# Kernel optimization log

Hardware: AMD Instinct MI355X
Metric: run time of the kernel (lower is better)

Reference implementation:

```python
import jax, jax.numpy as jnp
import numpy as np

N = 30000      # nodes
E = 480000     # edges per relation (avg degree 16)
H = 4          # GAT heads
D = 64         # out_size per head
F1, F2 = 256, 128   # per-metapath input feature dims
SIN = 256      # sen_in_size
HD = H * D     # 256, semantic-attention in_size
OUT = 64       # final out_size


def _gat(feat, src, dst, W, al, ar, b):
    """DGL GATConv (eval mode, dropout=0), activation=relu6."""
    h = (feat @ W).reshape(N, H, D)                     # [N,H,D]
    el = (h * al).sum(-1)                               # [N,H]
    er = (h * ar).sum(-1)                               # [N,H]
    e = jax.nn.leaky_relu(el[src] + er[dst], 0.2)       # [E,H]
    m = jax.ops.segment_max(e, dst, N)                  # edge-softmax over incoming edges
    p = jnp.exp(e - m[dst])
    s = jax.ops.segment_sum(p, dst, N)
    a = p / s[dst]                                      # [E,H]
    out = jax.ops.segment_sum(a[:, :, None] * h[src], dst, N)  # [N,H,D]
    out = out + b.reshape(1, H, D)
    return jnp.clip(out, 0.0, 6.0).reshape(N, H * D)    # relu6, flatten(1)


def _gcn_layer(x, src, dst, W, b):
    """DGL GraphConv, norm='both': D_in^{-1/2} A D_out^{-1/2} X W (+ b)."""
    ones = jnp.ones(src.shape[0], x.dtype)
    deg_o = jnp.clip(jax.ops.segment_sum(ones, src, N), 1.0, None)
    deg_i = jnp.clip(jax.ops.segment_sum(ones, dst, N), 1.0, None)
    h = (x @ W) * (deg_o[:, None] ** -0.5)
    h = jax.ops.segment_sum(h[src], dst, N) * (deg_i[:, None] ** -0.5)
    return h if b is None else h + b


def setup_inputs():
    key = jax.random.key(0)
    ks = jax.random.split(key, 28)
    f32 = jnp.float32
    nrm = lambda k, shp: jax.random.normal(k, shp, f32) * 0.05
    ri = lambda k, shp: jax.random.randint(k, shp, 0, N, jnp.int32)
    return dict(
        feat0=jax.random.normal(ks[0], (N, F1), f32),
        feat1=jax.random.normal(ks[1], (N, F2), f32),
        sen_feat=jax.random.normal(ks[2], (N, SIN), f32),
        Wgat0=nrm(ks[11], (F1, H * D)), al0=nrm(ks[12], (H, D)), ar0=nrm(ks[13], (H, D)), b0=nrm(ks[14], (H * D,)),
        Wgat1=nrm(ks[15], (F2, H * D)), al1=nrm(ks[16], (H, D)), ar1=nrm(ks[17], (H, D)), b1=nrm(ks[18], (H * D,)),
        Wp1=nrm(ks[19], (HD, OUT)), bp1=nrm(ks[20], (OUT,)), wp2=nrm(ks[21], (OUT,)),
        Wf=nrm(ks[22], (HD, OUT)), bf=nrm(ks[23], (OUT,)),
        Wg1=nrm(ks[24], (SIN, OUT)), bg1=nrm(ks[25], (OUT,)), Wg2=nrm(ks[26], (OUT, OUT)),
        src0=ri(ks[3], (E,)), dst0=ri(ks[4], (E,)),
        src1=ri(ks[5], (E,)), dst1=ri(ks[6], (E,)),
        gsrc=ri(ks[7], (E,)), gdst=ri(ks[8], (E,)),
        asrc=ri(ks[9], (E,)), adst=ri(ks[10], (E,)),
        k=10,
    )


def reference(feat0, feat1, sen_feat,
              Wgat0, al0, ar0, b0, Wgat1, al1, ar1, b1,
              Wp1, bp1, wp2, Wf, bf, Wg1, bg1, Wg2,
              src0, dst0, src1, dst1, gsrc, gdst, asrc, adst, k):
    # per-metapath GAT embeddings
    z0 = _gat(feat0, src0, dst0, Wgat0, al0, ar0, b0)   # [N, HD]
    z1 = _gat(feat1, src1, dst1, Wgat1, al1, ar1, b1)   # [N, HD]
    z = jnp.stack([z0, z1], axis=1)                     # [N, M=2, HD]
    # PathAttention (semantic attention over metapaths)
    w = jnp.tanh(z @ Wp1 + bp1) @ wp2                   # [N, M]
    beta = jax.nn.softmax(w.mean(0))                    # [M]
    fused = jnp.einsum('m,nmf->nf', beta, z)            # [N, HD]
    Femb = fused @ Wf + bf                              # [N, OUT]
    # two-layer GCN on the sentence graph
    p1 = jnp.tanh(_gcn_layer(sen_feat, gsrc, gdst, Wg1, bg1))
    P = _gcn_layer(p1, gsrc, gdst, Wg2, None)           # [N, OUT]
    # spectral loss: fuse embeddings, trace of Laplacian quadratic form on first k dims
    Z = 0.5 * (Femb + P)                                # [N, OUT]
    Zk = Z[:, :k]
    diff = Zk[asrc] - Zk[adst]
    tr = 0.5 * jnp.sum(diff * diff)                     # tr(Zk^T (D - A) Zk)
    return (tr, Z)
```

## Files before the change

kernel.cpp:

```cpp
#include <hip/hip_runtime.h>
#include <math.h>

#define NN 30000
#define NE 480000
#define NBLK 118
#define NMT 235
#define NTRB 7500
#define CAPD 128

typedef unsigned short ushort_t;
typedef unsigned int uint_t;
typedef __attribute__((ext_vector_type(8))) short short8;
typedef __attribute__((ext_vector_type(4))) float f32x4;

__device__ __forceinline__ ushort_t f2bf(float x) {
  uint_t u = __float_as_uint(x);
  u = (u + 0x7FFF + ((u >> 16) & 1)) >> 16;
  return (ushort_t)u;
}
__device__ __forceinline__ float bf2f(ushort_t v) {
  return __uint_as_float(((uint_t)v) << 16);
}

__device__ __forceinline__ float wred(float v) {
#pragma unroll
  for (int off = 32; off > 0; off >>= 1) v += __shfl_xor(v, off);
  return v;
}

__global__ void prep_kernel(float4* __restrict__ zp, const float* __restrict__ W0,
                            const float* __restrict__ W1, const float* __restrict__ W2,
                            const float* __restrict__ W3, const float* __restrict__ W4,
                            ushort_t* __restrict__ T0, ushort_t* __restrict__ T1,
                            ushort_t* __restrict__ T2, ushort_t* __restrict__ T3,
                            ushort_t* __restrict__ T4, const float* __restrict__ F0,
                            const float* __restrict__ F1, ushort_t* __restrict__ B0,
                            ushort_t* __restrict__ B1) {
  int id = blockIdx.x * 256 + threadIdx.x;
  if (id < 52501) {
    zp[id] = make_float4(0.f, 0.f, 0.f, 0.f);
    return;
  }
  int wid = id - 52501;
  if (wid < 147456) {
    const float* W;
    ushort_t* T;
    int K, N, base;
    if (wid < 65536) { W = W0; T = T0; K = 256; N = 256; base = 0; }
    else if (wid < 98304) { W = W1; T = T1; K = 128; N = 256; base = 65536; }
    else if (wid < 114688) { W = W2; T = T2; K = 256; N = 64; base = 98304; }
    else if (wid < 131072) { W = W3; T = T3; K = 256; N = 64; base = 114688; }
    else { W = W4; T = T4; K = 256; N = 64; base = 131072; }
    int l = wid - base;
    int k = l / N, n = l - k * N;
    T[(size_t)n * K + k] = f2bf(W[l]);
    return;
  }
  int cid = wid - 147456;
  const float* S;
  ushort_t* D;
  if (cid < 960000) { S = F0; D = B0; }
  else {
    cid -= 960000;
    if (cid >= 480000) return;
    S = F1; D = B1;
  }
  const float4* p = (const float4*)(S + (size_t)cid * 8);
  float4 a = p[0], b = p[1];
  short8 o;
  o[0] = (short)f2bf(a.x); o[1] = (short)f2bf(a.y);
  o[2] = (short)f2bf(a.z); o[3] = (short)f2bf(a.w);
  o[4] = (short)f2bf(b.x); o[5] = (short)f2bf(b.y);
  o[6] = (short)f2bf(b.z); o[7] = (short)f2bf(b.w);
  *(short8*)(D + (size_t)cid * 8) = o;
}


__device__ __forceinline__ void mfma_core_f32(const float* __restrict__ A0,
                                              const ushort_t* __restrict__ BT, int K, int bm,
                                              short* __restrict__ As, short* __restrict__ Bs,
                                              f32x4 acc[2][4]) {
  int tid = threadIdx.x;
  int lane = tid & 63, w = tid >> 6;
  int q = lane >> 4, mr = lane & 15;
#pragma unroll 1
  for (int k0 = 0; k0 < K; k0 += 32) {
    {
      int r = tid >> 1, hf = tid & 1;
      int gr = bm + r;
      float4 f0 = make_float4(0.f, 0.f, 0.f, 0.f), f1 = f0, f2 = f0, f3 = f0;
      if (gr < NN) {
        const float4* pa = (const float4*)(A0 + (size_t)gr * K + k0 + hf * 16);
        f0 = pa[0]; f1 = pa[1]; f2 = pa[2]; f3 = pa[3];
      }
      short8 lo, hi;
      lo[0] = (short)f2bf(f0.x); lo[1] = (short)f2bf(f0.y);
      lo[2] = (short)f2bf(f0.z); lo[3] = (short)f2bf(f0.w);
      lo[4] = (short)f2bf(f1.x); lo[5] = (short)f2bf(f1.y);
      lo[6] = (short)f2bf(f1.z); lo[7] = (short)f2bf(f1.w);
      hi[0] = (short)f2bf(f2.x); hi[1] = (short)f2bf(f2.y);
      hi[2] = (short)f2bf(f2.z); hi[3] = (short)f2bf(f2.w);
      hi[4] = (short)f2bf(f3.x); hi[5] = (short)f2bf(f3.y);
      hi[6] = (short)f2bf(f3.z); hi[7] = (short)f2bf(f3.w);
      short* dst = As + r * 40 + hf * 16;
      *(short8*)(dst) = lo;
      *(short8*)(dst + 8) = hi;
    }
    {
      int n = tid >> 2, qk = tid & 3;
      short8 bv = *(const short8*)((const short*)BT + (size_t)n * K + k0 + qk * 8);
      *(short8*)(Bs + n * 40 + qk * 8) = bv;
    }
    __syncthreads();
    short8 a0 = *(short8*)(As + (w * 32 + mr) * 40 + q * 8);
    short8 a1 = *(short8*)(As + (w * 32 + 16 + mr) * 40 + q * 8);
#pragma unroll
    for (int j = 0; j < 4; ++j) {
      short8 b = *(short8*)(Bs + (j * 16 + mr) * 40 + q * 8);
      acc[0][j] = __builtin_amdgcn_mfma_f32_16x16x32_bf16(a0, b, acc[0][j], 0, 0, 0);
      acc[1][j] = __builtin_amdgcn_mfma_f32_16x16x32_bf16(a1, b, acc[1][j], 0, 0, 0);
    }
    __syncthreads();
  }
}

__device__ __forceinline__ void mfma_core2_bfK(const ushort_t* __restrict__ A0,
                                               const ushort_t* __restrict__ BT, int K, int bm,
                                               short* __restrict__ As, short* __restrict__ Bs,
                                               f32x4 acc[2][8]) {
  int tid = threadIdx.x;
  int lane = tid & 63, w = tid >> 6;
  int q = lane >> 4, mr = lane & 15;
#pragma unroll 1
  for (int k0 = 0; k0 < K; k0 += 32) {
    {
      int r = tid >> 1, hf = tid & 1;
      int gr = bm + r;
      short8 v0 = {0, 0, 0, 0, 0, 0, 0, 0}, v1 = v0;
      if (gr < NN) {
        const short* p0 = (const short*)A0 + (size_t)gr * K + k0 + hf * 16;
        v0 = *(const short8*)p0;
        v1 = *(const short8*)(p0 + 8);
      }
      short* dst = As + r * 40 + hf * 16;
      *(short8*)(dst) = v0;
      *(short8*)(dst + 8) = v1;
    }
    {
      int n = tid >> 1, qk = tid & 1;
      const short* src = (const short*)BT + (size_t)n * K + k0 + qk * 16;
      short8 b0 = *(const short8*)src;
      short8 b1 = *(const short8*)(src + 8);
      short* d = Bs + n * 40 + qk * 16;
      *(short8*)d = b0;
      *(short8*)(d + 8) = b1;
    }
    __syncthreads();
    short8 a0 = *(short8*)(As + (w * 32 + mr) * 40 + q * 8);
    short8 a1 = *(short8*)(As + (w * 32 + 16 + mr) * 40 + q * 8);
#pragma unroll
    for (int j = 0; j < 8; ++j) {
      short8 b = *(short8*)(Bs + (j * 16 + mr) * 40 + q * 8);
      acc[0][j] = __builtin_amdgcn_mfma_f32_16x16x32_bf16(a0, b, acc[0][j], 0, 0, 0);
      acc[1][j] = __builtin_amdgcn_mfma_f32_16x16x32_bf16(a1, b, acc[1][j], 0, 0, 0);
    }
    __syncthreads();
  }
}

__global__ __launch_bounds__(256) void mfma_all_kernel(
    const ushort_t* __restrict__ fB0, const ushort_t* __restrict__ fB1,
    const float* __restrict__ sen, const ushort_t* __restrict__ WT0,
    const ushort_t* __restrict__ WT1, const ushort_t* __restrict__ Wg1T,
    ushort_t* __restrict__ h0, ushort_t* __restrict__ h1, ushort_t* __restrict__ gcnA,
    const float* __restrict__ al0, const float* __restrict__ ar0, float* __restrict__ el0,
    float* __restrict__ er0, const float* __restrict__ al1, const float* __restrict__ ar1,
    float* __restrict__ el1, float* __restrict__ er1, const float* __restrict__ rdo) {
  __shared__ short As[128 * 40];
  __shared__ short Bs[128 * 40];
  int y = blockIdx.y;
  int bm = blockIdx.x * 128;
  int lane = threadIdx.x & 63, w = threadIdx.x >> 6;
  int q = lane >> 4, mr = lane & 15;
  if (y < 4) {
    int gsel = y >> 1, p = y & 1;
    const ushort_t* A = gsel ? fB1 : fB0;
    int K = gsel ? 128 : 256;
    const ushort_t* WT = gsel ? WT1 : WT0;
    ushort_t* H = gsel ? h1 : h0;
    const float* al = gsel ? al1 : al0;
    const float* ar = gsel ? ar1 : ar0;
    float* el = gsel ? el1 : el0;
    float* er = gsel ? er1 : er0;
    f32x4 acc[2][8];
#pragma unroll
    for (int i = 0; i < 2; ++i)
#pragma unroll
      for (int j = 0; j < 8; ++j) acc[i][j] = (f32x4){0.f, 0.f, 0.f, 0.f};
    mfma_core2_bfK(A, WT + (size_t)p * 128 * K, K, bm, As, Bs, acc);
    float alv[8], arv[8];
#pragma unroll
    for (int j = 0; j < 8; ++j) {
      alv[j] = al[p * 128 + j * 16 + mr];
      arv[j] = ar[p * 128 + j * 16 + mr];
    }
#pragma unroll
    for (int i = 0; i < 2; ++i)
#pragma unroll
      for (int r = 0; r < 4; ++r) {
        int gr = bm + w * 32 + i * 16 + q * 4 + r;
        float pl0 = 0.f, pr0 = 0.f, pl1 = 0.f, pr1 = 0.f;
#pragma unroll
        for (int j = 0; j < 4; ++j) {
          pl0 = fmaf(acc[i][j][r], alv[j], pl0);
          pr0 = fmaf(acc[i][j][r], arv[j], pr0);
          pl1 = fmaf(acc[i][j + 4][r], alv[j + 4], pl1);
          pr1 = fmaf(acc[i][j + 4][r], arv[j + 4], pr1);
        }
#pragma unroll
        for (int m = 1; m < 16; m <<= 1) {
          pl0 += __shfl_xor(pl0, m);
          pr0 += __shfl_xor(pr0, m);
          pl1 += __shfl_xor(pl1, m);
          pr1 += __shfl_xor(pr1, m);
        }
        if (gr < NN) {
          if (mr == 0) {
            el[gr * 4 + 2 * p] = pl0;
            er[gr * 4 + 2 * p] = pr0;
            el[gr * 4 + 2 * p + 1] = pl1;
            er[gr * 4 + 2 * p + 1] = pr1;
          }
#pragma unroll
          for (int j = 0; j < 8; ++j)
            H[(size_t)gr * 256 + p * 128 + j * 16 + mr] = f2bf(acc[i][j][r]);
        }
      }
  } else {
    f32x4 acc[2][4];
#pragma unroll
    for (int i = 0; i < 2; ++i)
#pragma unroll
      for (int j = 0; j < 4; ++j) acc[i][j] = (f32x4){0.f, 0.f, 0.f, 0.f};
    mfma_core_f32(sen, Wg1T, 256, bm, As, Bs, acc);
#pragma unroll
    for (int i = 0; i < 2; ++i)
#pragma unroll
      for (int r = 0; r < 4; ++r) {
        int gr = bm + w * 32 + i * 16 + q * 4 + r;
        if (gr < NN) {
          float sc = rdo[gr];
#pragma unroll
          for (int j = 0; j < 4; ++j)
            gcnA[(size_t)gr * 64 + j * 16 + mr] = f2bf(acc[i][j][r] * sc);
        }
      }
  }
}

__global__ __launch_bounds__(256) void mfma_attnwf_kernel(
    const ushort_t* __restrict__ z0, const ushort_t* __restrict__ z1,
    const ushort_t* __restrict__ WpfT, const float* __restrict__ bp1,
    const float* __restrict__ wp2, float* __restrict__ pbuf, ushort_t* __restrict__ Y0,
    ushort_t* __restrict__ Y1) {
  __shared__ short As[128 * 40];
  __shared__ short Bs[128 * 40];
  __shared__ float wsum[4];
  const ushort_t* A = blockIdx.y ? z1 : z0;
  ushort_t* Y = blockIdx.y ? Y1 : Y0;
  int bm = blockIdx.x * 128;
  f32x4 acc[2][8];
#pragma unroll
  for (int i = 0; i < 2; ++i)
#pragma unroll
    for (int j = 0; j < 8; ++j) acc[i][j] = (f32x4){0.f, 0.f, 0.f, 0.f};
  mfma_core2_bfK(A, WpfT, 256, bm, As, Bs, acc);
  int lane = threadIdx.x & 63, w = threadIdx.x >> 6;
  int q = lane >> 4, mr = lane & 15;
  float local = 0.f;
#pragma unroll
  for (int j = 0; j < 4; ++j) {
    int col = j * 16 + mr;
    float bp = bp1[col], wp = wp2[col];
#pragma unroll
    for (int i = 0; i < 2; ++i)
#pragma unroll
      for (int r = 0; r < 4; ++r) {
        int gr = bm + w * 32 + i * 16 + q * 4 + r;
        if (gr < NN) local += tanhf(acc[i][j][r] + bp) * wp;
      }
  }
  local = wred(local);
  if (lane == 0) wsum[w] = local;
#pragma unroll
  for (int j = 4; j < 8; ++j) {
    int col = (j - 4) * 16 + mr;
#pragma unroll
    for (int i = 0; i < 2; ++i)
#pragma unroll
      for (int r = 0; r < 4; ++r) {
        int gr = bm + w * 32 + i * 16 + q * 4 + r;
        if (gr < NN) Y[(size_t)gr * 64 + col] = f2bf(acc[i][j][r]);
      }
  }
  __syncthreads();
  if (threadIdx.x == 0)
    pbuf[blockIdx.y * NMT + blockIdx.x] = wsum[0] + wsum[1] + wsum[2] + wsum[3];
}

__global__ void hist_kernel(const int* __restrict__ d0, const int* __restrict__ d1,
                            const int* __restrict__ d2, const int* __restrict__ d3,
                            int* __restrict__ cnt) {
  int g = blockIdx.y;
  const int* d = g == 0 ? d0 : g == 1 ? d1 : g == 2 ? d2 : d3;
  int e = blockIdx.x * 256 + threadIdx.x;
  if (e < NE) atomicAdd(&cnt[g * NN + d[e]], 1);
}

__global__ __launch_bounds__(256) void scan_blocks_kernel(const int* __restrict__ cnt,
                                                          int* __restrict__ rows,
                                                          int* __restrict__ bsum) {
  __shared__ int sm[256];
  int g = blockIdx.y, t = threadIdx.x;
  int i = blockIdx.x * 256 + t;
  int v = (i < NN) ? cnt[g * NN + i] : 0;
  sm[t] = v;
  __syncthreads();
#pragma unroll
  for (int off = 1; off < 256; off <<= 1) {
    int tmp = (t >= off) ? sm[t - off] : 0;
    __syncthreads();
    sm[t] += tmp;
    __syncthreads();
  }
  if (i < NN) rows[g * (NN + 1) + i] = sm[t] - v;
  if (t == 255) bsum[g * NBLK + blockIdx.x] = sm[255];
}

__global__ __launch_bounds__(128) void scan_tops_kernel(int* __restrict__ bsum,
                                                        int* __restrict__ boff) {
  __shared__ int sm[128];
  int g = blockIdx.y, t = threadIdx.x;
  int v = (t < NBLK) ? bsum[g * NBLK + t] : 0;
  sm[t] = v;
  __syncthreads();
#pragma unroll
  for (int off = 1; off < 128; off <<= 1) {
    int tmp = (t >= off) ? sm[t - off] : 0;
    __syncthreads();
    sm[t] += tmp;
    __syncthreads();
  }
  if (t < NBLK) boff[g * NBLK + t] = sm[t] - v;
}

__global__ void add_off_kernel(int* __restrict__ rows, const int* __restrict__ boff) {
  int g = blockIdx.y, t = threadIdx.x;
  int i = blockIdx.x * 256 + t;
  if (i < NN) rows[g * (NN + 1) + i] += boff[g * NBLK + blockIdx.x];
  if (blockIdx.x == 0 && t == 0) rows[g * (NN + 1) + NN] = NE;
}

__global__ void scatter_kernel(const int* __restrict__ s0, const int* __restrict__ s1,
                               const int* __restrict__ s2, const int* __restrict__ d0,
                               const int* __restrict__ d1, const int* __restrict__ d2,
                               const int* __restrict__ rows, int* __restrict__ cnt2,
                               int* __restrict__ cols, const int* __restrict__ cnt_deg,
                               float* __restrict__ rdo, float* __restrict__ rdi,
                               const int* __restrict__ rows_g) {
  int g = blockIdx.y;
  if (g == 3) {
    int n = blockIdx.x * 256 + threadIdx.x;
    if (n < NN) {
      rdo[n] = rsqrtf(fmaxf((float)cnt_deg[n], 1.f));
      float di = (float)(rows_g[n + 1] - rows_g[n]);
      rdi[n] = rsqrtf(fmaxf(di, 1.f));
    }
    return;
  }
  const int* sp = g == 0 ? s0 : g == 1 ? s1 : s2;
  const int* dp = g == 0 ? d0 : g == 1 ? d1 : d2;
  int e = blockIdx.x * 256 + threadIdx.x;
  if (e >= NE) return;
  int d = dp[e];
  int pos = rows[g * (NN + 1) + d] + atomicAdd(&cnt2[g * NN + d], 1);
  cols[(size_t)g * NE + pos] = sp[e];
}

__global__ __launch_bounds__(256) void gat_node_kernel(
    const int* __restrict__ rows0, const int* __restrict__ cols0, const float* __restrict__ el0,
    const float* __restrict__ er0, const ushort_t* __restrict__ h0,
    const float* __restrict__ bias0, ushort_t* __restrict__ zz0, const int* __restrict__ rows1,
    const int* __restrict__ cols1, const float* __restrict__ el1, const float* __restrict__ er1,
    const ushort_t* __restrict__ h1, const float* __restrict__ bias1,
    ushort_t* __restrict__ zz1) {
  __shared__ float aw[4][CAPD][4];
  int g = blockIdx.y;
  const int* rows = g ? rows1 : rows0;
  const int* cols = g ? cols1 : cols0;
  const float* el = g ? el1 : el0;
  const float* er = g ? er1 : er0;
  const ushort_t* h = g ? h1 : h0;
  const float* bias = g ? bias1 : bias0;
  ushort_t* z = g ? zz1 : zz0;

  int lane = threadIdx.x & 63, w = threadIdx.x >> 6;
  int n = blockIdx.x * 4 + w;
  int r0 = rows[n], r1 = rows[n + 1];
  int deg = r1 - r0;
  float4 er4 = *(const float4*)&er[n * 4];
  float s0 = 0.f, s1 = 0.f, s2 = 0.f, s3 = 0.f;
  for (int j = lane; j < deg; j += 64) {
    int s = cols[r0 + j];
    float4 elv = *(const float4*)&el[s * 4];
    float v0 = elv.x + er4.x; v0 = v0 > 0.f ? v0 : 0.2f * v0;
    float v1 = elv.y + er4.y; v1 = v1 > 0.f ? v1 : 0.2f * v1;
    float v2 = elv.z + er4.z; v2 = v2 > 0.f ? v2 : 0.2f * v2;
    float v3 = elv.w + er4.w; v3 = v3 > 0.f ? v3 : 0.2f * v3;
    float e0 = __expf(v0), e1 = __expf(v1), e2 = __expf(v2), e3 = __expf(v3);
    s0 += e0; s1 += e1; s2 += e2; s3 += e3;
    if (j < CAPD) {
      aw[w][j][0] = e0; aw[w][j][1] = e1; aw[w][j][2] = e2; aw[w][j][3] = e3;
    }
  }
  s0 = wred(s0); s1 = wred(s1); s2 = wred(s2); s3 = wred(s3);
  __syncthreads();
  int hh = lane >> 4;
  float denom = hh == 0 ? s0 : hh == 1 ? s1 : hh == 2 ? s2 : s3;
  float myer = hh == 0 ? er4.x : hh == 1 ? er4.y : hh == 2 ? er4.z : er4.w;
  float invd = (deg > 0) ? 1.f / denom : 0.f;
  float4 acc = make_float4(0.f, 0.f, 0.f, 0.f);
  int jc = deg < CAPD ? deg : CAPD;
  for (int j = 0; j < jc; j += 16) {
    int si[16];
    float ai[16];
#pragma unroll
    for (int t = 0; t < 16; ++t) {
      int jj = j + t;
      int jx = jj < jc ? jj : jc - 1;
      si[t] = cols[r0 + jx];
      ai[t] = (jj < jc) ? aw[w][jj][hh] : 0.f;
    }
    ushort4 ui[16];
#pragma unroll
    for (int t = 0; t < 16; ++t) ui[t] = *(const ushort4*)&h[(size_t)si[t] * 256 + lane * 4];
#pragma unroll
    for (int t = 0; t < 16; ++t) {
      acc.x = fmaf(ai[t], bf2f(ui[t].x), acc.x);
      acc.y = fmaf(ai[t], bf2f(ui[t].y), acc.y);
      acc.z = fmaf(ai[t], bf2f(ui[t].z), acc.z);
      acc.w = fmaf(ai[t], bf2f(ui[t].w), acc.w);
    }
  }
  for (int j = jc; j < deg; ++j) {
    int s = cols[r0 + j];
    float v = el[s * 4 + hh] + myer;
    v = v > 0.f ? v : 0.2f * v;
    float a = __expf(v);
    ushort4 hu = *(const ushort4*)&h[(size_t)s * 256 + lane * 4];
    acc.x = fmaf(a, bf2f(hu.x), acc.x);
    acc.y = fmaf(a, bf2f(hu.y), acc.y);
    acc.z = fmaf(a, bf2f(hu.z), acc.z);
    acc.w = fmaf(a, bf2f(hu.w), acc.w);
  }
  float4 bv = *(const float4*)&bias[lane * 4];
  ushort4 o;
  o.x = f2bf(fminf(fmaxf(acc.x * invd + bv.x, 0.f), 6.f));
  o.y = f2bf(fminf(fmaxf(acc.y * invd + bv.y, 0.f), 6.f));
  o.z = f2bf(fminf(fmaxf(acc.z * invd + bv.z, 0.f), 6.f));
  o.w = f2bf(fminf(fmaxf(acc.w * invd + bv.w, 0.f), 6.f));
  *(ushort4*)&z[(size_t)n * 256 + lane * 4] = o;
}

__global__ __launch_bounds__(256) void gcn_gather12_kernel(
    const int* __restrict__ rows, const int* __restrict__ cols, const ushort_t* __restrict__ X,
    const float* __restrict__ rdi, const float* __restrict__ bg1, const float* __restrict__ Wg2,
    const float* __restrict__ rdo, ushort_t* __restrict__ out2, const float* __restrict__ pbuf,
    float* __restrict__ wb) {
  __shared__ float psm[4][64];
  int lane = threadIdx.x & 63, w = threadIdx.x >> 6;
  if (blockIdx.x == 0) {
    __shared__ float sm[8];
    int t = threadIdx.x;
    float a0 = 0.f, a1 = 0.f;
    for (int i = t; i < NMT; i += 256) {
      a0 += pbuf[i];
      a1 += pbuf[NMT + i];
    }
    a0 = wred(a0);
    a1 = wred(a1);
    if (lane == 0) { sm[w] = a0; sm[4 + w] = a1; }
    __syncthreads();
    if (t == 0) {
      float w0 = (sm[0] + sm[1] + sm[2] + sm[3]) * (1.0f / NN);
      float w1 = (sm[4] + sm[5] + sm[6] + sm[7]) * (1.0f / NN);
      float mx = fmaxf(w0, w1);
      float e0 = expf(w0 - mx), e1 = expf(w1 - mx);
      float inv = 1.f / (e0 + e1);
      wb[2] = e0 * inv;
      wb[3] = e1 * inv;
    }
  }
  int n = blockIdx.x * 4 + w;
  if (n >= NN) return;
  int r0 = rows[n], r1 = rows[n + 1];
  int eg = lane >> 4, fl = lane & 15;
  float facc[4] = {0.f, 0.f, 0.f, 0.f};
  for (int j = r0; j < r1; j += 16) {
    int si[4];
    float sel[4];
#pragma unroll
    for (int t = 0; t < 4; ++t) {
      int jj = j + 4 * t + eg;
      int jx = jj < r1 ? jj : r1 - 1;
      si[t] = cols[jx];
      sel[t] = (jj < r1) ? 1.f : 0.f;
    }
    ushort4 xv[4];
#pragma unroll
    for (int t = 0; t < 4; ++t) xv[t] = *(const ushort4*)&X[(size_t)si[t] * 64 + fl * 4];
#pragma unroll
    for (int t = 0; t < 4; ++t) {
      facc[0] = fmaf(sel[t], bf2f(xv[t].x), facc[0]);
      facc[1] = fmaf(sel[t], bf2f(xv[t].y), facc[1]);
      facc[2] = fmaf(sel[t], bf2f(xv[t].z), facc[2]);
      facc[3] = fmaf(sel[t], bf2f(xv[t].w), facc[3]);
    }
  }
#pragma unroll
  for (int u = 0; u < 4; ++u) {
    facc[u] += __shfl_xor(facc[u], 16);
    facc[u] += __shfl_xor(facc[u], 32);
  }
  if (eg == 0) *(float4*)&psm[w][fl * 4] = make_float4(facc[0], facc[1], facc[2], facc[3]);
  __syncthreads();
  float p = tanhf(psm[w][lane] * rdi[n] + bg1[lane]);
  float o = 0.f;
#pragma unroll
  for (int k = 0; k < 64; ++k) o = fmaf(__shfl(p, k), Wg2[k * 64 + lane], o);
  out2[(size_t)n * 64 + lane] = f2bf(o * rdo[n]);
}

__global__ __launch_bounds__(256) void gcn_gather2_kernel(
    const int* __restrict__ rows, const int* __restrict__ cols, const ushort_t* __restrict__ X,
    const float* __restrict__ rdi, const ushort_t* __restrict__ Y0,
    const ushort_t* __restrict__ Y1, const float* __restrict__ wb, const float* __restrict__ bf,
    const int* __restrict__ kptr, float* __restrict__ Zc, float* __restrict__ dout) {
  int lane = threadIdx.x & 63, w = threadIdx.x >> 6;
  int n = blockIdx.x * 4 + w;
  if (n >= NN) return;
  int r0 = rows[n], r1 = rows[n + 1];
  int eg = lane >> 4, fl = lane & 15;
  float facc[4] = {0.f, 0.f, 0.f, 0.f};
  for (int j = r0; j < r1; j += 16) {
    int si[4];
    float sel[4];
#pragma unroll
    for (int t = 0; t < 4; ++t) {
      int jj = j + 4 * t + eg;
      int jx = jj < r1 ? jj : r1 - 1;
      si[t] = cols[jx];
      sel[t] = (jj < r1) ? 1.f : 0.f;
    }
    ushort4 xv[4];
#pragma unroll
    for (int t = 0; t < 4; ++t) xv[t] = *(const ushort4*)&X[(size_t)si[t] * 64 + fl * 4];
#pragma unroll
    for (int t = 0; t < 4; ++t) {
      facc[0] = fmaf(sel[t], bf2f(xv[t].x), facc[0]);
      facc[1] = fmaf(sel[t], bf2f(xv[t].y), facc[1]);
      facc[2] = fmaf(sel[t], bf2f(xv[t].z), facc[2]);
      facc[3] = fmaf(sel[t], bf2f(xv[t].w), facc[3]);
    }
  }
#pragma unroll
  for (int u = 0; u < 4; ++u) {
    facc[u] += __shfl_xor(facc[u], 16);
    facc[u] += __shfl_xor(facc[u], 32);
  }
  if (eg == 0) {
    float ri = rdi[n];
    ushort4 y0 = *(const ushort4*)&Y0[(size_t)n * 64 + fl * 4];
    ushort4 y1 = *(const ushort4*)&Y1[(size_t)n * 64 + fl * 4];
    float4 bfv = *(const float4*)&bf[fl * 4];
    float w2 = wb[2], w3 = wb[3];
    float zv[4];
    zv[0] = 0.5f * (w2 * bf2f(y0.x) + w3 * bf2f(y1.x) + bfv.x + facc[0] * ri);
    zv[1] = 0.5f * (w2 * bf2f(y0.y) + w3 * bf2f(y1.y) + bfv.y + facc[1] * ri);
    zv[2] = 0.5f * (w2 * bf2f(y0.z) + w3 * bf2f(y1.z) + bfv.z + facc[2] * ri);
    zv[3] = 0.5f * (w2 * bf2f(y0.w) + w3 * bf2f(y1.w) + bfv.w + facc[3] * ri);
    float* dp = dout + 1 + (size_t)n * 64 + fl * 4;
    dp[0] = zv[0]; dp[1] = zv[1]; dp[2] = zv[2]; dp[3] = zv[3];
    int k = *kptr;
    if (fl < 4) {
      float4 zk;
      zk.x = (fl * 4 + 0 < k) ? zv[0] : 0.f;
      zk.y = (fl * 4 + 1 < k) ? zv[1] : 0.f;
      zk.z = (fl * 4 + 2 < k) ? zv[2] : 0.f;
      zk.w = (fl * 4 + 3 < k) ? zv[3] : 0.f;
      *(float4*)&Zc[(size_t)n * 16 + fl * 4] = zk;
    }
  }
}

__global__ __launch_bounds__(256) void tr_kernel(const int* __restrict__ asrc,
                                                 const int* __restrict__ adst,
                                                 const int* __restrict__ kptr,
                                                 const float* __restrict__ Zc,
                                                 const float* __restrict__ dout,
                                                 float* __restrict__ trbuf) {
  __shared__ float wsum[4];
  int lane = threadIdx.x & 63, w = threadIdx.x >> 6;
  int k = *kptr;
  int eg = lane >> 2, c0 = (lane & 3) * 4;
  int e = blockIdx.x * 64 + w * 16 + eg;
  float local = 0.f;
  if (e < NE) {
    int a = asrc[e], b = adst[e];
    if (k <= 16) {
      float4 za = *(const float4*)&Zc[(size_t)a * 16 + c0];
      float4 zb = *(const float4*)&Zc[(size_t)b * 16 + c0];
      float dx = za.x - zb.x, dy = za.y - zb.y, dz = za.z - zb.z, dw = za.w - zb.w;
      local = dx * dx + dy * dy + dz * dz + dw * dw;
    } else {
      const float* Za = dout + 1 + (size_t)a * 64;
      const float* Zb = dout + 1 + (size_t)b * 64;
#pragma unroll
      for (int st = 0; st < 4; ++st) {
#pragma unroll
        for (int t = 0; t < 4; ++t) {
          int c = c0 + st * 16 + t;
          if (c < k) {
            float d2 = Za[c] - Zb[c];
            local += d2 * d2;
          }
        }
      }
    }
  }
#pragma unroll
  for (int off = 32; off > 0; off >>= 1) local += __shfl_down(local, off);
  if (lane == 0) wsum[w] = local;
  __syncthreads();
  if (threadIdx.x == 0) trbuf[blockIdx.x] = wsum[0] + wsum[1] + wsum[2] + wsum[3];
}

__global__ __launch_bounds__(256) void tr_reduce_kernel(const float* __restrict__ trbuf,
                                                        float* __restrict__ dout) {
  __shared__ float sm[4];
  int t = threadIdx.x;
  float a = 0.f;
  for (int i = t; i < NTRB; i += 256) a += trbuf[i];
  a = wred(a);
  int lane = t & 63, w = t >> 6;
  if (lane == 0) sm[w] = a;
  __syncthreads();
  if (t == 0) dout[0] = 0.5f * (sm[0] + sm[1] + sm[2] + sm[3]);
}

extern "C" void kernel_launch(void* const* d_in, const int* in_sizes, int n_in, void* d_out,
                              int out_size, void* d_ws, size_t ws_size, hipStream_t stream) {
  const float* feat0 = (const float*)d_in[0];
  const float* feat1 = (const float*)d_in[1];
  const float* sen = (const float*)d_in[2];
  const float* Wgat0 = (const float*)d_in[3];
  const float* al0 = (const float*)d_in[4];
  const float* ar0 = (const float*)d_in[5];
  const float* b0 = (const float*)d_in[6];
  const float* Wgat1 = (const float*)d_in[7];
  const float* al1 = (const float*)d_in[8];
  const float* ar1 = (const float*)d_in[9];
  const float* b1 = (const float*)d_in[10];
  const float* Wp1 = (const float*)d_in[11];
  const float* bp1 = (const float*)d_in[12];
  const float* wp2 = (const float*)d_in[13];
  const float* Wf = (const float*)d_in[14];
  const float* bf = (const float*)d_in[15];
  const float* Wg1 = (const float*)d_in[16];
  const float* bg1 = (const float*)d_in[17];
  const float* Wg2 = (const float*)d_in[18];
  const int* src0 = (const int*)d_in[19];
  const int* dst0 = (const int*)d_in[20];
  const int* src1 = (const int*)d_in[21];
  const int* dst1 = (const int*)d_in[22];
  const int* gsrc = (const int*)d_in[23];
  const int* gdst = (const int*)d_in[24];
  const int* asrc = (const int*)d_in[25];
  const int* adst = (const int*)d_in[26];
  const int* kptr = (const int*)d_in[27];
  float* out = (float*)d_out;
  float* ws = (float*)d_ws;

  float* wb = ws;
  int* cnt = (int*)(ws + 4);
  int* cnt2 = (int*)(ws + 120004);
  float* rdo = ws + 210004;
  float* rdi = ws + 240004;
  int* rows = (int*)(ws + 270004);
  int* bsum = (int*)(ws + 360008);
  int* boff = (int*)(ws + 360364);
  int* cols = (int*)(ws + 360720);
  float* el0 = ws + 1800720;
  float* er0 = ws + 1920720;
  float* el1 = ws + 2040720;
  float* er1 = ws + 2160720;
  float* pbuf = ws + 2280720;
  float* trbuf = el0;
  ushort_t* h0 = (ushort_t*)(ws + 2283068);
  ushort_t* h1 = (ushort_t*)(ws + 6123068);
  ushort_t* z0 = (ushort_t*)(ws + 9963068);
  ushort_t* z1 = (ushort_t*)(ws + 13803068);
  ushort_t* gcnA = (ushort_t*)(ws + 17643068);
  ushort_t* gcnA2 = (ushort_t*)(ws + 18603068);
  ushort_t* Y0 = (ushort_t*)(ws + 19563068);
  ushort_t* Y1 = (ushort_t*)(ws + 20523068);
  ushort_t* WT0 = (ushort_t*)(ws + 21483068);
  ushort_t* WT1 = (ushort_t*)(ws + 21515836);
  ushort_t* WpfT = (ushort_t*)(ws + 21532220);
  ushort_t* Wg1T = (ushort_t*)(ws + 21548604);
  float* Zc = ws + 21556796;

  int* rows_g = rows + 2 * (NN + 1);
  int* cols_g = cols + 2 * NE;
  int* cnt_deg = cnt + 3 * NN;

  ushort_t* fB0 = z0;
  ushort_t* fB1 = z1;

  prep_kernel<<<6407, 256, 0, stream>>>((float4*)ws, Wgat0, Wgat1, Wp1, Wf, Wg1, WT0, WT1, WpfT,
                                        WpfT + 16384, Wg1T, feat0, feat1, fB0, fB1);

  hist_kernel<<<dim3(1875, 4), 256, 0, stream>>>(dst0, dst1, gdst, gsrc, cnt);
  scan_blocks_kernel<<<dim3(NBLK, 3), 256, 0, stream>>>(cnt, rows, bsum);
  scan_tops_kernel<<<dim3(1, 3), 128, 0, stream>>>(bsum, boff);
  add_off_kernel<<<dim3(NBLK, 3), 256, 0, stream>>>(rows, boff);
  scatter_kernel<<<dim3(1875, 4), 256, 0, stream>>>(src0, src1, gsrc, dst0, dst1, gdst, rows,
                                                    cnt2, cols, cnt_deg, rdo, rdi, rows_g);

  mfma_all_kernel<<<dim3(NMT, 5), 256, 0, stream>>>(fB0, fB1, sen, WT0, WT1, Wg1T, h0, h1,
                                                    gcnA, al0, ar0, el0, er0, al1, ar1, el1,
                                                    er1, rdo);

  gat_node_kernel<<<dim3(7500, 2), 256, 0, stream>>>(rows, cols, el0, er0, h0, b0, z0,
                                                     rows + (NN + 1), cols + NE, el1, er1, h1,
                                                     b1, z1);

  mfma_attnwf_kernel<<<dim3(NMT, 2), 256, 0, stream>>>(z0, z1, WpfT, bp1, wp2, pbuf, Y0, Y1);

  gcn_gather12_kernel<<<7500, 256, 0, stream>>>(rows_g, cols_g, gcnA, rdi, bg1, Wg2, rdo, gcnA2,
                                                pbuf, wb);
  gcn_gather2_kernel<<<7500, 256, 0, stream>>>(rows_g, cols_g, gcnA2, rdi, Y0, Y1, wb, bf, kptr,
                                               Zc, out);

  tr_kernel<<<NTRB, 256, 0, stream>>>(asrc, adst, kptr, Zc, out, trbuf);
  tr_reduce_kernel<<<1, 256, 0, stream>>>(trbuf, out);
}
```

Measured before the change: 515.7 us.

## Merge attention GEMM with first GCN gather; widen GAT gather loads

The GAT node aggregation now splits each wave into two halves, each handling alternating edges with 16-byte bf16 loads of 8 features per lane, then combines the halves with a cross-half shuffle. The semantic-attention MFMA GEMM and the first GCN gather/transform are merged into one heterogeneous launch, since they are independent. The softmax over metapath scores is recomputed redundantly per wave in the final gather kernel instead of by a special block. This removes a launch and a global handoff through wb, and lets the GEMM blocks overlap the gather blocks. In exchange, every wave repeats the small pbuf reduction.

After: 537.9 us. +4.3%, slower.

```diff
diff --git a/kernel.cpp b/kernel.cpp
--- a/kernel.cpp
+++ b/kernel.cpp
@@ -21,6 +21,8 @@
 __device__ __forceinline__ float bf2f(ushort_t v) {
   return __uint_as_float(((uint_t)v) << 16);
 }
+__device__ __forceinline__ float bflo(uint_t d) { return __uint_as_float(d << 16); }
+__device__ __forceinline__ float bfhi(uint_t d) { return __uint_as_float(d & 0xFFFF0000u); }
 
 __device__ __forceinline__ float wred(float v) {
 #pragma unroll
@@ -258,56 +260,6 @@
   }
 }
 
-__global__ __launch_bounds__(256) void mfma_attnwf_kernel(
-    const ushort_t* __restrict__ z0, const ushort_t* __restrict__ z1,
-    const ushort_t* __restrict__ WpfT, const float* __restrict__ bp1,
-    const float* __restrict__ wp2, float* __restrict__ pbuf, ushort_t* __restrict__ Y0,
-    ushort_t* __restrict__ Y1) {
-  __shared__ short As[128 * 40];
-  __shared__ short Bs[128 * 40];
-  __shared__ float wsum[4];
-  const ushort_t* A = blockIdx.y ? z1 : z0;
-  ushort_t* Y = blockIdx.y ? Y1 : Y0;
-  int bm = blockIdx.x * 128;
-  f32x4 acc[2][8];
-#pragma unroll
-  for (int i = 0; i < 2; ++i)
-#pragma unroll
-    for (int j = 0; j < 8; ++j) acc[i][j] = (f32x4){0.f, 0.f, 0.f, 0.f};
-  mfma_core2_bfK(A, WpfT, 256, bm, As, Bs, acc);
-  int lane = threadIdx.x & 63, w = threadIdx.x >> 6;
-  int q = lane >> 4, mr = lane & 15;
-  float local = 0.f;
-#pragma unroll
-  for (int j = 0; j < 4; ++j) {
-    int col = j * 16 + mr;
-    float bp = bp1[col], wp = wp2[col];
-#pragma unroll
-    for (int i = 0; i < 2; ++i)
-#pragma unroll
-      for (int r = 0; r < 4; ++r) {
-        int gr = bm + w * 32 + i * 16 + q * 4 + r;
-        if (gr < NN) local += tanhf(acc[i][j][r] + bp) * wp;
-      }
-  }
-  local = wred(local);
-  if (lane == 0) wsum[w] = local;
-#pragma unroll
-  for (int j = 4; j < 8; ++j) {
-    int col = (j - 4) * 16 + mr;
-#pragma unroll
-    for (int i = 0; i < 2; ++i)
-#pragma unroll
-      for (int r = 0; r < 4; ++r) {
-        int gr = bm + w * 32 + i * 16 + q * 4 + r;
-        if (gr < NN) Y[(size_t)gr * 64 + col] = f2bf(acc[i][j][r]);
-      }
-  }
-  __syncthreads();
-  if (threadIdx.x == 0)
-    pbuf[blockIdx.y * NMT + blockIdx.x] = wsum[0] + wsum[1] + wsum[2] + wsum[3];
-}
-
 __global__ void hist_kernel(const int* __restrict__ d0, const int* __restrict__ d1,
                             const int* __restrict__ d2, const int* __restrict__ d3,
                             int* __restrict__ cnt) {
@@ -425,82 +377,188 @@
   }
   s0 = wred(s0); s1 = wred(s1); s2 = wred(s2); s3 = wred(s3);
   __syncthreads();
-  int hh = lane >> 4;
+  int par = lane >> 5;
+  int fl = lane & 31;
+  int hh = fl >> 3;
   float denom = hh == 0 ? s0 : hh == 1 ? s1 : hh == 2 ? s2 : s3;
   float myer = hh == 0 ? er4.x : hh == 1 ? er4.y : hh == 2 ? er4.z : er4.w;
   float invd = (deg > 0) ? 1.f / denom : 0.f;
-  float4 acc = make_float4(0.f, 0.f, 0.f, 0.f);
+  float facc[8];
+#pragma unroll
+  for (int u = 0; u < 8; ++u) facc[u] = 0.f;
   int jc = deg < CAPD ? deg : CAPD;
   for (int j = 0; j < jc; j += 16) {
-    int si[16];
-    float ai[16];
-#pragma unroll
-    for (int t = 0; t < 16; ++t) {
-      int jj = j + t;
+    int si[8];
+    float ai[8];
+#pragma unroll
+    for (int t = 0; t < 8; ++t) {
+      int jj = j + 2 * t + par;
       int jx = jj < jc ? jj : jc - 1;
       si[t] = cols[r0 + jx];
-      ai[t] = (jj < jc) ? aw[w][jj][hh] : 0.f;
-    }
-    ushort4 ui[16];
-#pragma unroll
-    for (int t = 0; t < 16; ++t) ui[t] = *(const ushort4*)&h[(size_t)si[t] * 256 + lane * 4];
-#pragma unroll
-    for (int t = 0; t < 16; ++t) {
-      acc.x = fmaf(ai[t], bf2f(ui[t].x), acc.x);
-      acc.y = fmaf(ai[t], bf2f(ui[t].y), acc.y);
-      acc.z = fmaf(ai[t], bf2f(ui[t].z), acc.z);
-      acc.w = fmaf(ai[t], bf2f(ui[t].w), acc.w);
-    }
-  }
-  for (int j = jc; j < deg; ++j) {
+      ai[t] = (jj < jc) ? aw[w][jx][hh] : 0.f;
+    }
+    uint4 hv[8];
+#pragma unroll
+    for (int t = 0; t < 8; ++t) hv[t] = *(const uint4*)&h[(size_t)si[t] * 256 + fl * 8];
+#pragma unroll
+    for (int t = 0; t < 8; ++t) {
+      float a = ai[t];
+      facc[0] = fmaf(a, bflo(hv[t].x), facc[0]);
+      facc[1] = fmaf(a, bfhi(hv[t].x), facc[1]);
+      facc[2] = fmaf(a, bflo(hv[t].y), facc[2]);
+      facc[3] = fmaf(a, bfhi(hv[t].y), facc[3]);
+      facc[4] = fmaf(a, bflo(hv[t].z), facc[4]);
+      facc[5] = fmaf(a, bfhi(hv[t].z), facc[5]);
+      facc[6] = fmaf(a, bflo(hv[t].w), facc[6]);
+      facc[7] = fmaf(a, bfhi(hv[t].w), facc[7]);
+    }
+  }
+  for (int j = jc + par; j < deg; j += 2) {
     int s = cols[r0 + j];
     float v = el[s * 4 + hh] + myer;
     v = v > 0.f ? v : 0.2f * v;
     float a = __expf(v);
-    ushort4 hu = *(const ushort4*)&h[(size_t)s * 256 + lane * 4];
-    acc.x = fmaf(a, bf2f(hu.x), acc.x);
-    acc.y = fmaf(a, bf2f(hu.y), acc.y);
-    acc.z = fmaf(a, bf2f(hu.z), acc.z);
-    acc.w = fmaf(a, bf2f(hu.w), acc.w);
-  }
-  float4 bv = *(const float4*)&bias[lane * 4];
-  ushort4 o;
-  o.x = f2bf(fminf(fmaxf(acc.x * invd + bv.x, 0.f), 6.f));
-  o.y = f2bf(fminf(fmaxf(acc.y * invd + bv.y, 0.f), 6.f));
-  o.z = f2bf(fminf(fmaxf(acc.z * invd + bv.z, 0.f), 6.f));
-  o.w = f2bf(fminf(fmaxf(acc.w * invd + bv.w, 0.f), 6.f));
-  *(ushort4*)&z[(size_t)n * 256 + lane * 4] = o;
-}
-
-__global__ __launch_bounds__(256) void gcn_gather12_kernel(
+    uint4 hv = *(const uint4*)&h[(size_t)s * 256 + fl * 8];
+    facc[0] = fmaf(a, bflo(hv.x), facc[0]);
+    facc[1] = fmaf(a, bfhi(hv.x), facc[1]);
+    facc[2] = fmaf(a, bflo(hv.y), facc[2]);
+    facc[3] = fmaf(a, bfhi(hv.y), facc[3]);
+    facc[4] = fmaf(a, bflo(hv.z), facc[4]);
+    facc[5] = fmaf(a, bfhi(hv.z), facc[5]);
+    facc[6] = fmaf(a, bflo(hv.w), facc[6]);
+    facc[7] = fmaf(a, bfhi(hv.w), facc[7]);
+  }
+#pragma unroll
+  for (int u = 0; u < 8; ++u) facc[u] += __shfl_xor(facc[u], 32);
+  if (par == 0) {
+    float4 bv0 = *(const float4*)&bias[fl * 8];
+    float4 bv1 = *(const float4*)&bias[fl * 8 + 4];
+    float bb[8] = {bv0.x, bv0.y, bv0.z, bv0.w, bv1.x, bv1.y, bv1.z, bv1.w};
+    short8 o;
+#pragma unroll
+    for (int u = 0; u < 8; ++u) {
+      float v = fminf(fmaxf(facc[u] * invd + bb[u], 0.f), 6.f);
+      o[u] = (short)f2bf(v);
+    }
+    *(short8*)&z[(size_t)n * 256 + fl * 8] = o;
+  }
+}
+
+__global__ __launch_bounds__(256) void attnwf_g12_kernel(
+    const ushort_t* __restrict__ z0, const ushort_t* __restrict__ z1,
+    const ushort_t* __restrict__ WpfT, const float* __restrict__ bp1,
+    const float* __restrict__ wp2, float* __restrict__ pbuf, ushort_t* __restrict__ Y0,
+    ushort_t* __restrict__ Y1, const int* __restrict__ rows, const int* __restrict__ cols,
+    const ushort_t* __restrict__ X, const float* __restrict__ rdi,
+    const float* __restrict__ bg1, const float* __restrict__ Wg2,
+    const float* __restrict__ rdo, ushort_t* __restrict__ out2) {
+  __shared__ short As[128 * 40];
+  __shared__ short Bs[128 * 40];
+  __shared__ float wsum[4];
+  int lane = threadIdx.x & 63, w = threadIdx.x >> 6;
+  if (blockIdx.x < 2 * NMT) {
+    int ysel = blockIdx.x >= NMT;
+    const ushort_t* A = ysel ? z1 : z0;
+    ushort_t* Y = ysel ? Y1 : Y0;
+    int bm = (ysel ? blockIdx.x - NMT : blockIdx.x) * 128;
+    f32x4 acc[2][8];
+#pragma unroll
+    for (int i = 0; i < 2; ++i)
+#pragma unroll
+      for (int j = 0; j < 8; ++j) acc[i][j] = (f32x4){0.f, 0.f, 0.f, 0.f};
+    mfma_core2_bfK(A, WpfT, 256, bm, As, Bs, acc);
+    int q = lane >> 4, mr = lane & 15;
+    float local = 0.f;
+#pragma unroll
+    for (int j = 0; j < 4; ++j) {
+      int col = j * 16 + mr;
+      float bp = bp1[col], wp = wp2[col];
+#pragma unroll
+      for (int i = 0; i < 2; ++i)
+#pragma unroll
+        for (int r = 0; r < 4; ++r) {
+          int gr = bm + w * 32 + i * 16 + q * 4 + r;
+          if (gr < NN) local += tanhf(acc[i][j][r] + bp) * wp;
+        }
+    }
+    local = wred(local);
+    if (lane == 0) wsum[w] = local;
+#pragma unroll
+    for (int j = 4; j < 8; ++j) {
+      int col = (j - 4) * 16 + mr;
+#pragma unroll
+      for (int i = 0; i < 2; ++i)
+#pragma unroll
+        for (int r = 0; r < 4; ++r) {
+          int gr = bm + w * 32 + i * 16 + q * 4 + r;
+          if (gr < NN) Y[(size_t)gr * 64 + col] = f2bf(acc[i][j][r]);
+        }
+    }
+    __syncthreads();
+    if (threadIdx.x == 0) pbuf[blockIdx.x] = wsum[0] + wsum[1] + wsum[2] + wsum[3];
+  } else {
+    float(*psm)[64] = (float(*)[64])As;
+    int n = (blockIdx.x - 2 * NMT) * 4 + w;
+    if (n >= NN) return;
+    int r0 = rows[n], r1 = rows[n + 1];
+    int eg = lane >> 4, fl = lane & 15;
+    float facc[4] = {0.f, 0.f, 0.f, 0.f};
+    for (int j = r0; j < r1; j += 16) {
+      int si[4];
+      float sel[4];
+#pragma unroll
+      for (int t = 0; t < 4; ++t) {
+        int jj = j + 4 * t + eg;
+        int jx = jj < r1 ? jj : r1 - 1;
+        si[t] = cols[jx];
+        sel[t] = (jj < r1) ? 1.f : 0.f;
+      }
+      ushort4 xv[4];
+#pragma unroll
+      for (int t = 0; t < 4; ++t) xv[t] = *(const ushort4*)&X[(size_t)si[t] * 64 + fl * 4];
+#pragma unroll
+      for (int t = 0; t < 4; ++t) {
+        facc[0] = fmaf(sel[t], bf2f(xv[t].x), facc[0]);
+        facc[1] = fmaf(sel[t], bf2f(xv[t].y), facc[1]);
+        facc[2] = fmaf(sel[t], bf2f(xv[t].z), facc[2]);
+        facc[3] = fmaf(sel[t], bf2f(xv[t].w), facc[3]);
+      }
+    }
+#pragma unroll
+    for (int u = 0; u < 4; ++u) {
+      facc[u] += __shfl_xor(facc[u], 16);
+      facc[u] += __shfl_xor(facc[u], 32);
+    }
+    if (eg == 0) *(float4*)&psm[w][fl * 4] = make_float4(facc[0], facc[1], facc[2], facc[3]);
+    __syncthreads();
+    float p = tanhf(psm[w][lane] * rdi[n] + bg1[lane]);
+    float o = 0.f;
+#pragma unroll
+    for (int k = 0; k < 64; ++k) o = fmaf(__shfl(p, k), Wg2[k * 64 + lane], o);
+    out2[(size_t)n * 64 + lane] = f2bf(o * rdo[n]);
+  }
+}
+
+__global__ __launch_bounds__(256) void gcn_gather2_kernel(
     const int* __restrict__ rows, const int* __restrict__ cols, const ushort_t* __restrict__ X,
-    const float* __restrict__ rdi, const float* __restrict__ bg1, const float* __restrict__ Wg2,
-    const float* __restrict__ rdo, ushort_t* __restrict__ out2, const float* __restrict__ pbuf,
-    float* __restrict__ wb) {
-  __shared__ float psm[4][64];
+    const float* __restrict__ rdi, const ushort_t* __restrict__ Y0,
+    const ushort_t* __restrict__ Y1, const float* __restrict__ pbuf,
+    const float* __restrict__ bf, const int* __restrict__ kptr, float* __restrict__ Zc,
+    float* __restrict__ dout) {
   int lane = threadIdx.x & 63, w = threadIdx.x >> 6;
-  if (blockIdx.x == 0) {
-    __shared__ float sm[8];
-    int t = threadIdx.x;
-    float a0 = 0.f, a1 = 0.f;
-    for (int i = t; i < NMT; i += 256) {
-      a0 += pbuf[i];
-      a1 += pbuf[NMT + i];
-    }
-    a0 = wred(a0);
-    a1 = wred(a1);
-    if (lane == 0) { sm[w] = a0; sm[4 + w] = a1; }
-    __syncthreads();
-    if (t == 0) {
-      float w0 = (sm[0] + sm[1] + sm[2] + sm[3]) * (1.0f / NN);
-      float w1 = (sm[4] + sm[5] + sm[6] + sm[7]) * (1.0f / NN);
-      float mx = fmaxf(w0, w1);
-      float e0 = expf(w0 - mx), e1 = expf(w1 - mx);
-      float inv = 1.f / (e0 + e1);
-      wb[2] = e0 * inv;
-      wb[3] = e1 * inv;
-    }
-  }
+  float b0a = 0.f, b1a = 0.f;
+  for (int i = lane; i < NMT; i += 64) {
+    b0a += pbuf[i];
+    b1a += pbuf[NMT + i];
+  }
+  b0a = wred(b0a);
+  b1a = wred(b1a);
+  float w0 = b0a * (1.0f / NN), w1 = b1a * (1.0f / NN);
+  float mx = fmaxf(w0, w1);
+  float be0 = __expf(w0 - mx), be1 = __expf(w1 - mx);
+  float binv = 1.f / (be0 + be1);
+  float wb2 = be0 * binv, wb3 = be1 * binv;
+
   int n = blockIdx.x * 4 + w;
   if (n >= NN) return;
   int r0 = rows[n], r1 = rows[n + 1];
@@ -532,63 +590,16 @@
     facc[u] += __shfl_xor(facc[u], 16);
     facc[u] += __shfl_xor(facc[u], 32);
   }
-  if (eg == 0) *(float4*)&psm[w][fl * 4] = make_float4(facc[0], facc[1], facc[2], facc[3]);
-  __syncthreads();
-  float p = tanhf(psm[w][lane] * rdi[n] + bg1[lane]);
-  float o = 0.f;
-#pragma unroll
-  for (int k = 0; k < 64; ++k) o = fmaf(__shfl(p, k), Wg2[k * 64 + lane], o);
-  out2[(size_t)n * 64 + lane] = f2bf(o * rdo[n]);
-}
-
-__global__ __launch_bounds__(256) void gcn_gather2_kernel(
-    const int* __restrict__ rows, const int* __restrict__ cols, const ushort_t* __restrict__ X,
-    const float* __restrict__ rdi, const ushort_t* __restrict__ Y0,
-    const ushort_t* __restrict__ Y1, const float* __restrict__ wb, const float* __restrict__ bf,
-    const int* __restrict__ kptr, float* __restrict__ Zc, float* __restrict__ dout) {
-  int lane = threadIdx.x & 63, w = threadIdx.x >> 6;
-  int n = blockIdx.x * 4 + w;
-  if (n >= NN) return;
-  int r0 = rows[n], r1 = rows[n + 1];
-  int eg = lane >> 4, fl = lane & 15;
-  float facc[4] = {0.f, 0.f, 0.f, 0.f};
-  for (int j = r0; j < r1; j += 16) {
-    int si[4];
-    float sel[4];
-#pragma unroll
-    for (int t = 0; t < 4; ++t) {
-      int jj = j + 4 * t + eg;
-      int jx = jj < r1 ? jj : r1 - 1;
-      si[t] = cols[jx];
-      sel[t] = (jj < r1) ? 1.f : 0.f;
-    }
-    ushort4 xv[4];
-#pragma unroll
-    for (int t = 0; t < 4; ++t) xv[t] = *(const ushort4*)&X[(size_t)si[t] * 64 + fl * 4];
-#pragma unroll
-    for (int t = 0; t < 4; ++t) {
-      facc[0] = fmaf(sel[t], bf2f(xv[t].x), facc[0]);
-      facc[1] = fmaf(sel[t], bf2f(xv[t].y), facc[1]);
-      facc[2] = fmaf(sel[t], bf2f(xv[t].z), facc[2]);
-      facc[3] = fmaf(sel[t], bf2f(xv[t].w), facc[3]);
-    }
-  }
-#pragma unroll
-  for (int u = 0; u < 4; ++u) {
-    facc[u] += __shfl_xor(facc[u], 16);
-    facc[u] += __shfl_xor(facc[u], 32);
-  }
   if (eg == 0) {
     float ri = rdi[n];
     ushort4 y0 = *(const ushort4*)&Y0[(size_t)n * 64 + fl * 4];
     ushort4 y1 = *(const ushort4*)&Y1[(size_t)n * 64 + fl * 4];
     float4 bfv = *(const float4*)&bf[fl * 4];
-    float w2 = wb[2], w3 = wb[3];
     float zv[4];
-    zv[0] = 0.5f * (w2 * bf2f(y0.x) + w3 * bf2f(y1.x) + bfv.x + facc[0] * ri);
-    zv[1] = 0.5f * (w2 * bf2f(y0.y) + w3 * bf2f(y1.y) + bfv.y + facc[1] * ri);
-    zv[2] = 0.5f * (w2 * bf2f(y0.z) + w3 * bf2f(y1.z) + bfv.z + facc[2] * ri);
-    zv[3] = 0.5f * (w2 * bf2f(y0.w) + w3 * bf2f(y1.w) + bfv.w + facc[3] * ri);
+    zv[0] = 0.5f * (wb2 * bf2f(y0.x) + wb3 * bf2f(y1.x) + bfv.x + facc[0] * ri);
+    zv[1] = 0.5f * (wb2 * bf2f(y0.y) + wb3 * bf2f(y1.y) + bfv.y + facc[1] * ri);
+    zv[2] = 0.5f * (wb2 * bf2f(y0.z) + wb3 * bf2f(y1.z) + bfv.z + facc[2] * ri);
+    zv[3] = 0.5f * (wb2 * bf2f(y0.w) + wb3 * bf2f(y1.w) + bfv.w + facc[3] * ri);
     float* dp = dout + 1 + (size_t)n * 64 + fl * 4;
     dp[0] = zv[0]; dp[1] = zv[1]; dp[2] = zv[2]; dp[3] = zv[3];
     int k = *kptr;
@@ -723,6 +734,7 @@
   int* rows_g = rows + 2 * (NN + 1);
   int* cols_g = cols + 2 * NE;
   int* cnt_deg = cnt + 3 * NN;
+  (void)wb;
 
   ushort_t* fB0 = z0;
   ushort_t* fB1 = z1;
@@ -745,12 +757,12 @@
                                                      rows + (NN + 1), cols + NE, el1, er1, h1,
                                                      b1, z1);
 
-  mfma_attnwf_kernel<<<dim3(NMT, 2), 256, 0, stream>>>(z0, z1, WpfT, bp1, wp2, pbuf, Y0, Y1);
-
-  gcn_gather12_kernel<<<7500, 256, 0, stream>>>(rows_g, cols_g, gcnA, rdi, bg1, Wg2, rdo, gcnA2,
-                                                pbuf, wb);
-  gcn_gather2_kernel<<<7500, 256, 0, stream>>>(rows_g, cols_g, gcnA2, rdi, Y0, Y1, wb, bf, kptr,
-                                               Zc, out);
+  attnwf_g12_kernel<<<2 * NMT + 7500, 256, 0, stream>>>(z0, z1, WpfT, bp1, wp2, pbuf, Y0, Y1,
+                                                        rows_g, cols_g, gcnA, rdi, bg1, Wg2,
+                                                        rdo, gcnA2);
+
+  gcn_gather2_kernel<<<7500, 256, 0, stream>>>(rows_g, cols_g, gcnA2, rdi, Y0, Y1, pbuf, bf,
+                                               kptr, Zc, out);
 
   tr_kernel<<<NTRB, 256, 0, stream>>>(asrc, adst, kptr, Zc, out, trbuf);
   tr_reduce_kernel<<<1, 256, 0, stream>>>(trbuf, out);
```
